# Kernel tuning notes

Measured on AMD Instinct MI355X. Metric: run time of the kernel, lower is better.

Reference implementation:

```python
import jax, jax.numpy as jnp
import numpy as np

DN = ('NCHW', 'OIHW', 'NCHW')

def conv2d(x, w, b, stride, pad):
    y = jax.lax.conv_general_dilated(x, w, (stride, stride), ((pad, pad), (pad, pad)), dimension_numbers=DN)
    return y + b[None, :, None, None]

def convt2d(x, w, b):
    # torch ConvTranspose2d(k=4, stride=2, padding=1); torch weight layout [Cin, Cout, kH, kW]
    wf = jnp.flip(w, (2, 3)).transpose(1, 0, 2, 3)  # -> [Cout, Cin, kH, kW]
    y = jax.lax.conv_general_dilated(x, wf, (1, 1), ((2, 2), (2, 2)), lhs_dilation=(2, 2), dimension_numbers=DN)
    return y + b[None, :, None, None]

def setup_inputs() -> dict:
    key = jax.random.key(0)
    ks = jax.random.split(key, 20)
    Hc, E, K = 128, 256, 8192
    s = lambda k, shape, fan: jax.random.normal(k, shape, jnp.float32) * (1.0 / np.sqrt(fan))
    inp = {
        'x': jax.random.normal(ks[0], (4, 3, 256, 256), jnp.float32),
        'enc_w1': s(ks[1], (Hc, 3, 4, 4), 3 * 16), 'enc_b1': jnp.zeros((Hc,), jnp.float32),
        'enc_w2': s(ks[2], (Hc, Hc, 4, 4), Hc * 16), 'enc_b2': jnp.zeros((Hc,), jnp.float32),
        'enc_w3': s(ks[3], (Hc, Hc, 3, 3), Hc * 9), 'enc_b3': jnp.zeros((Hc,), jnp.float32),
        'qconv_w': s(ks[4], (E, Hc, 1, 1), Hc), 'qconv_b': jnp.zeros((E,), jnp.float32),
        'codebook': jax.random.uniform(ks[5], (K, E), jnp.float32, -1.0 / K, 1.0 / K),
        'pqconv_w': s(ks[6], (Hc, E, 1, 1), E), 'pqconv_b': jnp.zeros((Hc,), jnp.float32),
        'dec_w1': s(ks[7], (Hc, Hc, 3, 3), Hc * 9), 'dec_b1': jnp.zeros((Hc,), jnp.float32),
        'dect_w2': s(ks[8], (Hc, Hc, 4, 4), Hc * 16), 'dect_b2': jnp.zeros((Hc,), jnp.float32),
        'dect_w3': s(ks[9], (Hc, 3, 4, 4), Hc * 16), 'dect_b3': jnp.zeros((3,), jnp.float32),
    }
    return inp

def quantize(z, codebook):
    B, C, H, W = z.shape
    zf = z.transpose(0, 2, 3, 1).reshape(-1, C)  # [N, C]
    d = (jnp.sum(zf * zf, axis=1, keepdims=True)
         + jnp.sum(codebook * codebook, axis=1)
         - 2.0 * zf @ codebook.T)  # [N, K]
    indices = jnp.argmin(d, axis=1)
    quant = codebook[indices].reshape(B, H, W, C).transpose(0, 3, 1, 2)
    commit_loss = jnp.mean((jax.lax.stop_gradient(quant) - z) ** 2)
    quant = z + jax.lax.stop_gradient(quant - z)  # straight-through
    return quant, indices, commit_loss

def reference(x, enc_w1, enc_b1, enc_w2, enc_b2, enc_w3, enc_b3, qconv_w, qconv_b,
              codebook, pqconv_w, pqconv_b, dec_w1, dec_b1, dect_w2, dect_b2, dect_w3, dect_b3):
    h = jax.nn.relu(conv2d(x, enc_w1, enc_b1, 2, 1))
    h = jax.nn.relu(conv2d(h, enc_w2, enc_b2, 2, 1))
    h = conv2d(h, enc_w3, enc_b3, 1, 1)
    h = conv2d(h, qconv_w, qconv_b, 1, 0)
    quant, indices, commit_loss = quantize(h, codebook)
    q = conv2d(quant, pqconv_w, pqconv_b, 1, 0)
    d = jax.nn.relu(conv2d(q, dec_w1, dec_b1, 1, 1))
    d = jax.nn.relu(convt2d(d, dect_w2, dect_b2))
    recon = convt2d(d, dect_w3, dect_b3)
    return recon, commit_loss, indices
```

## Files before the change

kernel.cpp:

```cpp
#include <hip/hip_runtime.h>

#define OFF_A     ((size_t)0)
#define OFF_BINFO ((size_t)8388608)
#define OFF_B     ((size_t)34611200)
#define OFF_C     ((size_t)43532288)
#define OFF_D     ((size_t)52453376)
#define OFF_E     ((size_t)69230592)
#define OFF_ZN    ((size_t)81813504)
#define OFF_CN    ((size_t)81879040)
#define OFF_IDX   ((size_t)81911808)
#define OFF_ACC   ((size_t)81977344)
#define OFF_WR2   ((size_t)81977600)
#define OFF_WR3   ((size_t)83026176)
#define OFF_QWT   ((size_t)83050752)
#define OFF_WD2   ((size_t)83181824)
#define OFF_WD3   ((size_t)85278976)
#define OFF_WD1   ((size_t)86458624)

#define VQ_MARGIN 1.2e-4f
#define LDSS 40

typedef __attribute__((ext_vector_type(8))) _Float16 f16x8;
typedef __attribute__((ext_vector_type(4))) float f32x4;

__device__ __forceinline__ unsigned fkey(float f) {
  unsigned u = __float_as_uint(f);
  return (u & 0x80000000u) ? ~u : (u | 0x80000000u);
}
__device__ __forceinline__ float funkey(unsigned k) {
  unsigned u = (k & 0x80000000u) ? (k ^ 0x80000000u) : ~k;
  return __uint_as_float(u);
}
__device__ __forceinline__ void padzero_img(float* base, int S, int t) {
  for (int e = t; e < 4 * S - 4; e += 256) {
    int rr, cc;
    if (e < S) { rr = 0; cc = e; }
    else if (e < 2 * S) { rr = S - 1; cc = e - S; }
    else { rr = ((e - 2 * S) >> 1) + 1; cc = (e & 1) ? (S - 1) : 0; }
    base[rr * S + cc] = 0.0f;
  }
}
__device__ __forceinline__ void padzero_img_h(_Float16* base, int S, int t) {
  for (int e = t; e < 4 * S - 4; e += 256) {
    int rr, cc;
    if (e < S) { rr = 0; cc = e; }
    else if (e < 2 * S) { rr = S - 1; cc = e - S; }
    else { rr = ((e - 2 * S) >> 1) + 1; cc = (e & 1) ? (S - 1) : 0; }
    base[rr * S + cc] = (_Float16)0.0f;
  }
}

__global__ __launch_bounds__(256) void prep_k(
    const float* __restrict__ dtw2, _Float16* __restrict__ wh2,
    const float* __restrict__ dtw3, float* __restrict__ wr3,
    const float* __restrict__ qw,   float* __restrict__ qwT,
    const float* __restrict__ ew2,  double* __restrict__ wd2,
    const float* __restrict__ ew3,  double* __restrict__ wd3,
    const float* __restrict__ ew1,  double* __restrict__ wd1,
    float* __restrict__ xpad, float* __restrict__ h1p, float* __restrict__ h2p) {
  int b = blockIdx.x, t = threadIdx.x;
  if (b < 256) {
    int tid = b * 256 + t;
    int ci = tid & 127, co = (tid >> 7) & 127, cls = tid >> 14;
    int kh0 = 1 - (cls >> 1), kw0 = 1 - (cls & 1);
    const float* s = dtw2 + ((size_t)ci * 128 + co) * 16;
    _Float16* d = wh2 + (size_t)tid * 4;
    float d0 = s[kh0 * 4 + kw0];       float d1v = s[kh0 * 4 + kw0 + 2];
    float d2v = s[(kh0 + 2) * 4 + kw0]; float d3v = s[(kh0 + 2) * 4 + kw0 + 2];
    d[0] = (_Float16)d1v; d[1] = (_Float16)d0;
    d[2] = (_Float16)d3v; d[3] = (_Float16)d2v;
  } else if (b < 262) {
    int tid = (b - 256) * 256 + t;
    if (tid < 1536) {
      int ci = tid & 127, co = (tid >> 7) % 3, cls = tid / 384;
      int kh0 = 1 - (cls >> 1), kw0 = 1 - (cls & 1);
      const float* s = dtw3 + ((size_t)ci * 3 + co) * 16;
      float* d = wr3 + (size_t)tid * 4;
      d[0] = s[kh0 * 4 + kw0];       d[1] = s[kh0 * 4 + kw0 + 2];
      d[2] = s[(kh0 + 2) * 4 + kw0]; d[3] = s[(kh0 + 2) * 4 + kw0 + 2];
    }
  } else if (b < 390) {
    int tid = (b - 262) * 256 + t;
    int co = tid & 255, ci = tid >> 8;
    qwT[(size_t)ci * 256 + co] = qw[(size_t)co * 128 + ci];
  } else if (b < 1414) {
    int tid = (b - 390) * 256 + t;
    wd2[tid] = (double)ew2[tid];
  } else if (b < 1990) {
    int tid = (b - 1414) * 256 + t;
    wd3[tid] = (double)ew3[tid];
  } else if (b < 2014) {
    int tid = (b - 1990) * 256 + t;
    wd1[tid] = (double)ew1[tid];
  } else if (b < 2026) {
    padzero_img(xpad + (size_t)(b - 2014) * 66564, 258, t);
  } else if (b < 2538) {
    padzero_img(h1p + (size_t)(b - 2026) * 16900, 130, t);
  } else {
    padzero_img(h2p + (size_t)(b - 2538) * 4356, 66, t);
  }
}

__global__ __launch_bounds__(256) void padx_k(const float* __restrict__ x,
                                              float* __restrict__ xp) {
  int tid = blockIdx.x * 256 + threadIdx.x;
  int wo = tid & 255, ho = (tid >> 8) & 255, c = tid >> 16;
  xp[((size_t)c * 258 + ho + 1) * 258 + wo + 1] = x[tid];
}

__global__ __launch_bounds__(256) void conv1_k(
    const float* __restrict__ xp, const double* __restrict__ wd,
    const float* __restrict__ bias, float* __restrict__ h1p) {
  int b = blockIdx.x;
  int chunk = b & 63, cog = (b >> 6) & 15, n = b >> 10;
  int t = threadIdx.x;
  int wo = t & 127, ho = chunk * 2 + (t >> 7);
  int co0 = cog * 8;
  const float* xb = xp + (size_t)n * 3 * 66564 + (size_t)(2 * ho) * 258 + 2 * wo;
  double acc[8] = {};
  for (int ci = 0; ci < 3; ++ci) {
    const float* xc = xb + (size_t)ci * 66564;
    float cf[16];
#pragma unroll
    for (int kh = 0; kh < 4; ++kh)
#pragma unroll
      for (int kw = 0; kw < 4; ++kw) cf[kh * 4 + kw] = xc[kh * 258 + kw];
    const double* wp = wd + (size_t)co0 * 48 + ci * 16;
#pragma unroll
    for (int tp = 0; tp < 16; ++tp) {
      double xd = (double)cf[tp];
#pragma unroll
      for (int cc = 0; cc < 8; ++cc)
        acc[cc] = fma(xd, wp[(size_t)cc * 48 + tp], acc[cc]);
    }
  }
#pragma unroll
  for (int cc = 0; cc < 8; ++cc) {
    float r = (float)((double)bias[co0 + cc] + acc[cc]);
    h1p[(((size_t)n * 128 + co0 + cc) * 130 + ho + 1) * 130 + wo + 1] = fmaxf(r, 0.0f);
  }
}

__global__ __launch_bounds__(256) void conv2_k(
    const float* __restrict__ h1p, const double* __restrict__ wd,
    const float* __restrict__ bias, float* __restrict__ h2p) {
  int b = blockIdx.x;
  int chunk = b & 15, cog = (b >> 4) & 15, n = b >> 8;
  int t = threadIdx.x;
  int wo = t & 63, ho = chunk * 4 + (t >> 6);
  int co0 = cog * 8;
  const float* xb = h1p + (size_t)n * 128 * 16900 + (size_t)(2 * ho) * 130 + 2 * wo;
  double acc[8] = {};
  for (int ci = 0; ci < 128; ++ci) {
    const float* xc = xb + (size_t)ci * 16900;
    float cf[16];
#pragma unroll
    for (int kh = 0; kh < 4; ++kh) {
      float2 p0 = *(const float2*)(xc + kh * 130);
      float2 p1 = *(const float2*)(xc + kh * 130 + 2);
      cf[kh * 4 + 0] = p0.x; cf[kh * 4 + 1] = p0.y;
      cf[kh * 4 + 2] = p1.x; cf[kh * 4 + 3] = p1.y;
    }
    const double* wp = wd + (size_t)co0 * 2048 + ci * 16;
#pragma unroll
    for (int tp = 0; tp < 16; ++tp) {
      double xd = (double)cf[tp];
#pragma unroll
      for (int cc = 0; cc < 8; ++cc)
        acc[cc] = fma(xd, wp[(size_t)cc * 2048 + tp], acc[cc]);
    }
  }
#pragma unroll
  for (int cc = 0; cc < 8; ++cc) {
    float r = (float)((double)bias[co0 + cc] + acc[cc]);
    h2p[(((size_t)n * 128 + co0 + cc) * 66 + ho + 1) * 66 + wo + 1] = fmaxf(r, 0.0f);
  }
}

__global__ __launch_bounds__(256) void conv3_k(
    const float* __restrict__ h2p, const double* __restrict__ wd,
    const float* __restrict__ bias, float* __restrict__ h3) {
  int b = blockIdx.x;
  int chunk = b & 15, cog = (b >> 4) & 15, n = b >> 8;
  int t = threadIdx.x;
  int wo = t & 63, ho = chunk * 4 + (t >> 6);
  int co0 = cog * 8;
  const float* xb = h2p + (size_t)n * 128 * 4356 + (size_t)ho * 66 + wo;
  double acc[8] = {};
  for (int ci = 0; ci < 128; ++ci) {
    const float* xc = xb + (size_t)ci * 4356;
    float cf[9];
#pragma unroll
    for (int kh = 0; kh < 3; ++kh)
#pragma unroll
      for (int kw = 0; kw < 3; ++kw) cf[kh * 3 + kw] = xc[kh * 66 + kw];
    const double* wp = wd + (size_t)co0 * 1152 + ci * 9;
#pragma unroll
    for (int tp = 0; tp < 9; ++tp) {
      double xd = (double)cf[tp];
#pragma unroll
      for (int cc = 0; cc < 8; ++cc)
        acc[cc] = fma(xd, wp[(size_t)cc * 1152 + tp], acc[cc]);
    }
  }
#pragma unroll
  for (int cc = 0; cc < 8; ++cc)
    h3[(((size_t)n * 128 + co0 + cc) << 12) + (ho << 6) + wo] =
        (float)((double)bias[co0 + cc] + acc[cc]);
}

__global__ __launch_bounds__(256) void qconv_z_k(
    const float* __restrict__ h3, const float* __restrict__ wT,
    const float* __restrict__ bias, float* __restrict__ zf,
    _Float16* __restrict__ Ap, float* __restrict__ znb) {
  __shared__ double wsum[4];
  int p  = blockIdx.x;
  int co = threadIdx.x;
  int n  = p >> 12;
  int hw = p & 4095;
  const float* xp = h3 + ((size_t)n * 128) * 4096 + hw;
  double a[4] = {0.0, 0.0, 0.0, 0.0};
  for (int ci = 0; ci < 128; ci += 4) {
#pragma unroll
    for (int u = 0; u < 4; ++u) {
      float xv = xp[(size_t)(ci + u) * 4096];
      a[u] = fma((double)xv, (double)wT[(size_t)(ci + u) * 256 + co], a[u]);
    }
  }
  double acc = (double)bias[co] + ((a[0] + a[1]) + (a[2] + a[3]));
  float zv = (float)acc;
  zf[(size_t)p * 256 + co] = zv;
  Ap[(size_t)p * 256 + co] = (_Float16)zv;
  float xx = zv * zv;
  double s = (double)xx;
#pragma unroll
  for (int off = 32; off > 0; off >>= 1) s += __shfl_down(s, off, 64);
  if ((co & 63) == 0) wsum[co >> 6] = s;
  __syncthreads();
  if (co == 0) znb[p] = (float)((wsum[0] + wsum[1]) + (wsum[2] + wsum[3]));
}

__global__ __launch_bounds__(256) void cbprep_k(
    const float* __restrict__ cb, _Float16* __restrict__ Bp,
    float* __restrict__ cnb) {
  __shared__ double wsum[4];
  int k = blockIdx.x, t = threadIdx.x;
  float c = cb[(size_t)k * 256 + t];
  Bp[(size_t)k * 256 + t] = (_Float16)(c * 512.0f);
  float xx = c * c;
  double s = (double)xx;
#pragma unroll
  for (int off = 32; off > 0; off >>= 1) s += __shfl_down(s, off, 64);
  if ((t & 63) == 0) wsum[t >> 6] = s;
  __syncthreads();
  if (t == 0) cnb[k] = (float)((wsum[0] + wsum[1]) + (wsum[2] + wsum[3]));
}

__global__ __launch_bounds__(256, 2) void vq_gemm_k(
    const _Float16* __restrict__ Ah, const _Float16* __restrict__ Bh,
    const float* __restrict__ cnArr, int4* __restrict__ binfo) {
  __shared__ __align__(16) _Float16 As[128 * LDSS];
  __shared__ __align__(16) _Float16 Bs[128 * LDSS];
  __shared__ unsigned loc[128];
  __shared__ int cnt_sh[128];
  __shared__ int cand_sh[128][2];
  const int t = threadIdx.x;
  const int w = t >> 6, L = t & 63;
  const int mb = blockIdx.x >> 6;
  const int nb = blockIdx.x & 63;
  const int m0 = mb << 7, n0 = nb << 7;
  if (t < 128) { loc[t] = 0xFFFFFFFFu; cnt_sh[t] = 0; }
  f32x4 acc[4][4] = {};
  const int wr = (w >> 1) << 6, wc = (w & 1) << 6;
  const int srow = L >> 2, kg = L & 3;
  const int q = L >> 4, ln = L & 15;
  for (int kk = 0; kk < 256; kk += 32) {
    __syncthreads();
#pragma unroll
    for (int c = 0; c < 2; ++c) {
      const int row = (w << 5) + (c << 4) + srow;
      const f16x8 av = *(const f16x8*)(Ah + (size_t)(m0 + row) * 256 + kk + kg * 8);
      *(f16x8*)(&As[row * LDSS + kg * 8]) = av;
      const f16x8 bv = *(const f16x8*)(Bh + (size_t)(n0 + row) * 256 + kk + kg * 8);
      *(f16x8*)(&Bs[row * LDSS + kg * 8]) = bv;
    }
    __syncthreads();
    f16x8 af[4], bf[4];
#pragma unroll
    for (int i = 0; i < 4; ++i)
      af[i] = *(const f16x8*)(&As[(wr + 16 * i + ln) * LDSS + q * 8]);
#pragma unroll
    for (int j = 0; j < 4; ++j)
      bf[j] = *(const f16x8*)(&Bs[(wc + 16 * j + ln) * LDSS + q * 8]);
#pragma unroll
    for (int i = 0; i < 4; ++i)
#pragma unroll
      for (int j = 0; j < 4; ++j)
        acc[i][j] = __builtin_amdgcn_mfma_f32_16x16x32_f16(af[i], bf[j], acc[i][j], 0, 0, 0);
  }
  float cnv[4];
#pragma unroll
  for (int j = 0; j < 4; ++j) cnv[j] = cnArr[n0 + wc + 16 * j + ln];
#pragma unroll
  for (int i = 0; i < 4; ++i)
#pragma unroll
    for (int r = 0; r < 4; ++r) {
      float mn = 3.4e38f;
#pragma unroll
      for (int j = 0; j < 4; ++j)
        mn = fminf(mn, fmaf(-0.00390625f, acc[i][j][r], cnv[j]));
#pragma unroll
      for (int s = 1; s < 16; s <<= 1)
        mn = fminf(mn, __shfl_xor(mn, s, 64));
      if (ln == 0) atomicMin(&loc[wr + 16 * i + 4 * q + r], fkey(mn));
    }
  __syncthreads();
#pragma unroll
  for (int i = 0; i < 4; ++i)
#pragma unroll
    for (int r = 0; r < 4; ++r) {
      const int rib = wr + 16 * i + 4 * q + r;
      const float thr = funkey(loc[rib]) + VQ_MARGIN;
#pragma unroll
      for (int j = 0; j < 4; ++j) {
        float s = fmaf(-0.00390625f, acc[i][j][r], cnv[j]);
        if (s <= thr) {
          int slot = atomicAdd(&cnt_sh[rib], 1);
          if (slot < 2) cand_sh[rib][slot] = n0 + wc + 16 * j + ln;
        }
      }
    }
  __syncthreads();
  if (t < 128) {
    int4 v;
    v.x = cnt_sh[t];
    v.y = cand_sh[t][0];
    v.z = cand_sh[t][1];
    v.w = (int)__float_as_uint(funkey(loc[t]));
    binfo[(size_t)(m0 + t) * 64 + nb] = v;
  }
}

__global__ __launch_bounds__(256) void vq_phase3_k(
    const float* __restrict__ zf, const float* __restrict__ cb,
    const float* __restrict__ znArr, const float* __restrict__ cnArr,
    const int4* __restrict__ binfo, int* __restrict__ idxOut,
    float* __restrict__ accum) {
  if (blockIdx.x == 0 && threadIdx.x == 0) *accum = 0.0f;
  const int lane = threadIdx.x & 63;
  const int r = blockIdx.x * 4 + (threadIdx.x >> 6);
  const float* zr = zf + (size_t)r * 256;
  double z4[4];
#pragma unroll
  for (int j = 0; j < 4; ++j) z4[j] = (double)zr[lane + (j << 6)];
  const float znr = znArr[r];
  int4 b = binfo[(size_t)r * 64 + lane];
  float bv = __uint_as_float((unsigned)b.w);
  float m = bv;
#pragma unroll
  for (int off = 32; off > 0; off >>= 1) m = fminf(m, __shfl_down(m, off, 64));
  m = __shfl(m, 0, 64);
  const float thr = m + VQ_MARGIN;
  unsigned long long mask = __ballot(bv <= thr);
  float bestd = 3.4e38f;
  int bestk = 0x7fffffff;
  while (mask) {
    const int nb = (int)__builtin_ctzll(mask);
    mask &= mask - 1;
    const int c  = __shfl(b.x, nb, 64);
    const int k0 = __shfl(b.y, nb, 64);
    const int k1 = __shfl(b.z, nb, 64);
    const int nsc = (c <= 2) ? c : 128;
    for (int s2 = 0; s2 < nsc; ++s2) {
      const int k = (c <= 2) ? (s2 == 0 ? k0 : k1) : (nb * 128 + s2);
      const float* ck = cb + (size_t)k * 256;
      double p = 0.0;
#pragma unroll
      for (int j = 0; j < 4; ++j)
        p = fma(z4[j], (double)ck[lane + (j << 6)], p);
#pragma unroll
      for (int off = 32; off > 0; off >>= 1) p += __shfl_down(p, off, 64);
      if (lane == 0) {
        float mm2 = (float)(2.0 * p);
        float t1 = znr + cnArr[k];
        float d = t1 - mm2;
        if (d < bestd || (d == bestd && k < bestk)) { bestd = d; bestk = k; }
      }
    }
  }
  if (lane == 0) idxOut[r] = bestk;
}

__global__ __launch_bounds__(256) void commit_k(
    const float* __restrict__ zf, const float* __restrict__ cb,
    const int* __restrict__ idxArr, float* __restrict__ accum,
    float* __restrict__ outIdxF) {
  __shared__ float wsum[4];
  const int p = blockIdx.x;
  const int t = threadIdx.x;
  const int k = idxArr[p];
  float d = cb[(size_t)k * 256 + t] - zf[(size_t)p * 256 + t];
  float v = d * d;
#pragma unroll
  for (int off = 32; off > 0; off >>= 1) v += __shfl_down(v, off, 64);
  if ((t & 63) == 0) wsum[t >> 6] = v;
  __syncthreads();
  if (t == 0) {
    atomicAdd(accum, wsum[0] + wsum[1] + wsum[2] + wsum[3]);
    outIdxF[p] = (float)k;
  }
}

__global__ __launch_bounds__(256) void pc_k(const float* __restrict__ cb,
                                            const float* __restrict__ pw,
                                            float* __restrict__ PC) {
  int tid = blockIdx.x * 256 + threadIdx.x;
  int co = tid & 127, k = tid >> 7;
  const float* c = cb + (size_t)k * 256;
  const float* w = pw + (size_t)co * 256;
  float a0 = 0.0f, a1 = 0.0f, a2 = 0.0f, a3 = 0.0f;
  for (int ci = 0; ci < 256; ci += 4) {
    a0 = fmaf(c[ci], w[ci], a0);
    a1 = fmaf(c[ci + 1], w[ci + 1], a1);
    a2 = fmaf(c[ci + 2], w[ci + 2], a2);
    a3 = fmaf(c[ci + 3], w[ci + 3], a3);
  }
  PC[tid] = (a0 + a1) + (a2 + a3);
}

__global__ __launch_bounds__(256) void padzero_dec_k(
    float* __restrict__ qbufp, _Float16* __restrict__ d1pH,
    float* __restrict__ d2p) {
  int b = blockIdx.x, t = threadIdx.x;
  if (b < 512)       padzero_img(qbufp + (size_t)b * 4356, 66, t);
  else if (b < 1024) padzero_img_h(d1pH + (size_t)(b - 512) * 4356, 66, t);
  else               padzero_img(d2p + (size_t)(b - 1024) * 16900, 130, t);
}

__global__ __launch_bounds__(256) void gather_pc_k(
    const float* __restrict__ PC, const int* __restrict__ idxArr,
    const float* __restrict__ pb, float* __restrict__ qp) {
  int tid = blockIdx.x * 256 + threadIdx.x;
  int hw = tid & 4095;
  int co = (tid >> 12) & 127;
  int n  = tid >> 19;
  int p  = (n << 12) + hw;
  int h = hw >> 6, w2 = hw & 63;
  qp[(((size_t)n * 128 + co) * 66 + h + 1) * 66 + w2 + 1] =
      PC[(size_t)idxArr[p] * 128 + co] + pb[co];
}

__global__ __launch_bounds__(256) void dconv1_k(
    const float* __restrict__ qp, const float* __restrict__ w,
    const float* __restrict__ bias, _Float16* __restrict__ d1pH) {
  int b = blockIdx.x;
  int chunk = b & 15, cog = (b >> 4) & 15, n = b >> 8;
  int t = threadIdx.x;
  int wo = t & 63, ho = chunk * 4 + (t >> 6);
  int co0 = cog * 8;
  const float* xb = qp + (size_t)n * 128 * 4356 + (size_t)ho * 66 + wo;
  float acc[8] = {};
  for (int ci = 0; ci < 128; ++ci) {
    const float* xc = xb + (size_t)ci * 4356;
    float xv[9];
#pragma unroll
    for (int kh = 0; kh < 3; ++kh)
#pragma unroll
      for (int kw = 0; kw < 3; ++kw) xv[kh * 3 + kw] = xc[kh * 66 + kw];
#pragma unroll
    for (int cc = 0; cc < 8; ++cc) {
      const float* wp = w + (size_t)(co0 + cc) * 1152 + ci * 9;
#pragma unroll
      for (int tp = 0; tp < 9; ++tp)
        acc[cc] = fmaf(xv[tp], wp[tp], acc[cc]);
    }
  }
#pragma unroll
  for (int cc = 0; cc < 8; ++cc)
    d1pH[(((size_t)n * 128 + co0 + cc) * 66 + ho + 1) * 66 + wo + 1] =
        (_Float16)fmaxf(bias[co0 + cc] + acc[cc], 0.0f);
}

__global__ __launch_bounds__(256) void convt2_k(
    const _Float16* __restrict__ xh, const _Float16* __restrict__ wh,
    const float* __restrict__ bias, float* __restrict__ y) {
  int b = blockIdx.x;
  int i = b & 63, cog = (b >> 6) & 7, cls = (b >> 9) & 3, n = b >> 11;
  int cph = cls >> 1, cpw = cls & 1;
  int t = threadIdx.x;
  int wv = t >> 6, l = t & 63;
  int q = l >> 4, ln = l & 15;
  int wb = (wv << 4) + ln;
  int co0 = cog << 4;
  int r0 = i + 1 + cph, r1 = r0 - 1;
  int c1 = wb + cpw;
  int o0 = r0 * 66 + c1, o1 = r1 * 66 + c1;
  const unsigned short* xb =
      (const unsigned short*)xh + (size_t)n * 128 * 4356 + (size_t)(q * 2) * 4356;
  const _Float16* ap = wh + (size_t)(cls * 128 + co0 + ln) * 512 + q * 8;
  f32x4 acc = {0.0f, 0.0f, 0.0f, 0.0f};
  for (int s = 0; s < 16; ++s) {
    const unsigned short* pa = xb + (size_t)(s * 8) * 4356;
    const unsigned short* pb2 = pa + 4356;
    unsigned v0 = pa[o0], v1 = pa[o0 + 1];
    unsigned v2 = pa[o1], v3 = pa[o1 + 1];
    unsigned v4 = pb2[o0], v5 = pb2[o0 + 1];
    unsigned v6 = pb2[o1], v7 = pb2[o1 + 1];
    union { unsigned u[4]; f16x8 h; } bb;
    bb.u[0] = v0 | (v1 << 16);
    bb.u[1] = v2 | (v3 << 16);
    bb.u[2] = v4 | (v5 << 16);
    bb.u[3] = v6 | (v7 << 16);
    const f16x8 af = *(const f16x8*)(ap + s * 32);
    acc = __builtin_amdgcn_mfma_f32_16x16x32_f16(af, bb.h, acc, 0, 0, 0);
  }
  int ho = 2 * i + cph, wo = 2 * wb + cpw;
#pragma unroll
  for (int r = 0; r < 4; ++r) {
    int co = co0 + q * 4 + r;
    y[(((size_t)n * 128 + co) * 130 + ho + 1) * 130 + wo + 1] =
        fmaxf(bias[co] + acc[r], 0.0f);
  }
}

__global__ __launch_bounds__(256) void convt3_k(
    const float* __restrict__ xp, const float* __restrict__ wr,
    const float* __restrict__ bias, float* __restrict__ y,
    const float* __restrict__ accum, float* __restrict__ outLoss) {
  int b = blockIdx.x;
  if (b == 0 && threadIdx.x == 0) *outLoss = *accum * (1.0f / 4194304.0f);
  int chunk = b & 63, cls = (b >> 6) & 3, n = b >> 8;
  int cph = cls >> 1, cpw = cls & 1;
  int t = threadIdx.x;
  int wb = t & 127, i = chunk * 2 + (t >> 7);
  int ho = 2 * i + cph, wo = 2 * wb + cpw;
  int r0 = i + 1 + cph, r1 = r0 - 1;
  int c0 = wb + 1 + cpw, c1 = c0 - 1;
  const float* xb = xp + (size_t)n * 128 * 16900;
  float acc[3] = {0.0f, 0.0f, 0.0f};
  for (int ci = 0; ci < 128; ++ci) {
    const float* xc = xb + (size_t)ci * 16900;
    float x00 = xc[r0 * 130 + c0], x01 = xc[r0 * 130 + c1];
    float x10 = xc[r1 * 130 + c0], x11 = xc[r1 * 130 + c1];
#pragma unroll
    for (int cc = 0; cc < 3; ++cc) {
      const float* w4 = wr + (((size_t)cls * 3 + cc) * 128 + ci) * 4;
      acc[cc] = fmaf(x00, w4[0], acc[cc]);
      acc[cc] = fmaf(x01, w4[1], acc[cc]);
      acc[cc] = fmaf(x10, w4[2], acc[cc]);
      acc[cc] = fmaf(x11, w4[3], acc[cc]);
    }
  }
#pragma unroll
  for (int cc = 0; cc < 3; ++cc)
    y[(((size_t)n * 3 + cc) << 16) + (ho << 8) + wo] = bias[cc] + acc[cc];
}

extern "C" void kernel_launch(void* const* d_in, const int* in_sizes, int n_in,
                              void* d_out, int out_size, void* d_ws, size_t ws_size,
                              hipStream_t stream) {
  const float* x    = (const float*)d_in[0];
  const float* ew1  = (const float*)d_in[1];
  const float* eb1  = (const float*)d_in[2];
  const float* ew2  = (const float*)d_in[3];
  const float* eb2  = (const float*)d_in[4];
  const float* ew3  = (const float*)d_in[5];
  const float* eb3  = (const float*)d_in[6];
  const float* qw   = (const float*)d_in[7];
  const float* qb   = (const float*)d_in[8];
  const float* cb   = (const float*)d_in[9];
  const float* pw   = (const float*)d_in[10];
  const float* pb   = (const float*)d_in[11];
  const float* dw1  = (const float*)d_in[12];
  const float* db1  = (const float*)d_in[13];
  const float* dtw2 = (const float*)d_in[14];
  const float* dtb2 = (const float*)d_in[15];
  const float* dtw3 = (const float*)d_in[16];
  const float* dtb3 = (const float*)d_in[17];

  char* wsb = (char*)d_ws;
  float*    h1p  = (float*)(wsb + OFF_A);
  _Float16* Ap   = (_Float16*)(wsb + OFF_A);
  int4*     binfo= (int4*)(wsb + OFF_BINFO);
  float*    d2p  = (float*)(wsb + OFF_A);
  float*    h2p  = (float*)(wsb + OFF_B);
  float*    qbufp= (float*)(wsb + OFF_B);
  float*    xpad = (float*)(wsb + OFF_C);
  float*    h3   = (float*)(wsb + OFF_C);
  _Float16* d1pH = (_Float16*)(wsb + OFF_C);
  float*    zff  = (float*)(wsb + OFF_D);
  _Float16* Bp   = (_Float16*)(wsb + OFF_E);
  float*    PC   = (float*)(wsb + OFF_E);
  float*    znb  = (float*)(wsb + OFF_ZN);
  float*    cnb  = (float*)(wsb + OFF_CN);
  int*      idxb = (int*)(wsb + OFF_IDX);
  float*    accum= (float*)(wsb + OFF_ACC);
  _Float16* wh2  = (_Float16*)(wsb + OFF_WR2);
  float*    wr3  = (float*)(wsb + OFF_WR3);
  float*    qwT  = (float*)(wsb + OFF_QWT);
  double*   wd2  = (double*)(wsb + OFF_WD2);
  double*   wd3  = (double*)(wsb + OFF_WD3);
  double*   wd1  = (double*)(wsb + OFF_WD1);

  float* out      = (float*)d_out;
  float* outLoss  = out + 786432;
  float* outIdxF  = out + 786433;

  hipLaunchKernelGGL(prep_k, dim3(3050), dim3(256), 0, stream,
                     dtw2, wh2, dtw3, wr3, qw, qwT, ew2, wd2, ew3, wd3,
                     ew1, wd1, xpad, h1p, h2p);

  hipLaunchKernelGGL(padx_k,    dim3(3072),  dim3(256), 0, stream, x, xpad);
  hipLaunchKernelGGL(conv1_k,   dim3(4096),  dim3(256), 0, stream, xpad, wd1, eb1, h1p);
  hipLaunchKernelGGL(conv2_k,   dim3(1024),  dim3(256), 0, stream, h1p, wd2, eb2, h2p);
  hipLaunchKernelGGL(conv3_k,   dim3(1024),  dim3(256), 0, stream, h2p, wd3, eb3, h3);
  hipLaunchKernelGGL(qconv_z_k, dim3(16384), dim3(256), 0, stream, h3, qwT, qb, zff, Ap, znb);

  hipLaunchKernelGGL(cbprep_k,    dim3(8192),  dim3(256), 0, stream, cb, Bp, cnb);
  hipLaunchKernelGGL(vq_gemm_k,   dim3(8192),  dim3(256), 0, stream, Ap, Bp, cnb, binfo);
  hipLaunchKernelGGL(vq_phase3_k, dim3(4096),  dim3(256), 0, stream, zff, cb, znb, cnb, binfo, idxb, accum);
  hipLaunchKernelGGL(commit_k,    dim3(16384), dim3(256), 0, stream, zff, cb, idxb, accum, outIdxF);

  hipLaunchKernelGGL(pc_k,          dim3(4096), dim3(256), 0, stream, cb, pw, PC);
  hipLaunchKernelGGL(padzero_dec_k, dim3(1536), dim3(256), 0, stream, qbufp, d1pH, d2p);
  hipLaunchKernelGGL(gather_pc_k,   dim3(8192), dim3(256), 0, stream, PC, idxb, pb, qbufp);
  hipLaunchKernelGGL(dconv1_k,      dim3(1024), dim3(256), 0, stream, qbufp, dw1, db1, d1pH);
  hipLaunchKernelGGL(convt2_k,      dim3(8192), dim3(256), 0, stream, d1pH, wh2, dtb2, d2p);
  hipLaunchKernelGGL(convt3_k,      dim3(1024), dim3(256), 0, stream, d2p, wr3, dtb3, out, accum, outLoss);
}
```

Before: 1.387 ms.

## Run decoder 3x3 conv on fp16 MFMA and store decoder activations in fp16

Rewrites the decoder 3x3 conv (dconv1) from a scalar fp32 FMA loop into an implicit-GEMM kernel using 16x16x32 fp16 MFMA. Its weights are pre-rearranged into an fp16 tap-major layout inside the prep kernel. The quantized input and the first transposed-conv output now use fp16 buffers, which halves the memory traffic for gather, convt2 and convt3. The cost is lower precision in the decoder path, and the MFMA B-operand is built from eight strided 16-bit loads per step.

After: 1.338 ms. -3.5%, faster.

```diff
diff --git a/kernel.cpp b/kernel.cpp
--- a/kernel.cpp
+++ b/kernel.cpp
@@ -11,6 +11,7 @@
 #define OFF_IDX   ((size_t)81911808)
 #define OFF_ACC   ((size_t)81977344)
 #define OFF_WR2   ((size_t)81977600)
+#define OFF_WHD1  ((size_t)82501888)
 #define OFF_WR3   ((size_t)83026176)
 #define OFF_QWT   ((size_t)83050752)
 #define OFF_WD2   ((size_t)83181824)
@@ -57,6 +58,7 @@
     const float* __restrict__ ew2,  double* __restrict__ wd2,
     const float* __restrict__ ew3,  double* __restrict__ wd3,
     const float* __restrict__ ew1,  double* __restrict__ wd1,
+    const float* __restrict__ dw1,  _Float16* __restrict__ whd1,
     float* __restrict__ xpad, float* __restrict__ h1p, float* __restrict__ h2p) {
   int b = blockIdx.x, t = threadIdx.x;
   if (b < 256) {
@@ -96,8 +98,13 @@
     padzero_img(xpad + (size_t)(b - 2014) * 66564, 258, t);
   } else if (b < 2538) {
     padzero_img(h1p + (size_t)(b - 2026) * 16900, 130, t);
+  } else if (b < 3050) {
+    padzero_img(h2p + (size_t)(b - 2538) * 4356, 66, t);
   } else {
-    padzero_img(h2p + (size_t)(b - 2538) * 4356, 66, t);
+    int tid = (b - 3050) * 256 + t;
+    int co = tid / 1152, k = tid - co * 1152;
+    int tap = k >> 7, ci = k & 127;
+    whd1[tid] = (_Float16)dw1[((size_t)co * 128 + ci) * 9 + tap];
   }
 }
 
@@ -429,61 +436,68 @@
 }
 
 __global__ __launch_bounds__(256) void padzero_dec_k(
-    float* __restrict__ qbufp, _Float16* __restrict__ d1pH,
-    float* __restrict__ d2p) {
+    _Float16* __restrict__ qH, _Float16* __restrict__ d1pH,
+    _Float16* __restrict__ d2pH) {
   int b = blockIdx.x, t = threadIdx.x;
-  if (b < 512)       padzero_img(qbufp + (size_t)b * 4356, 66, t);
+  if (b < 512)       padzero_img_h(qH + (size_t)b * 4356, 66, t);
   else if (b < 1024) padzero_img_h(d1pH + (size_t)(b - 512) * 4356, 66, t);
-  else               padzero_img(d2p + (size_t)(b - 1024) * 16900, 130, t);
+  else               padzero_img_h(d2pH + (size_t)(b - 1024) * 16900, 130, t);
 }
 
 __global__ __launch_bounds__(256) void gather_pc_k(
     const float* __restrict__ PC, const int* __restrict__ idxArr,
-    const float* __restrict__ pb, float* __restrict__ qp) {
+    const float* __restrict__ pb, _Float16* __restrict__ qH) {
   int tid = blockIdx.x * 256 + threadIdx.x;
   int hw = tid & 4095;
   int co = (tid >> 12) & 127;
   int n  = tid >> 19;
   int p  = (n << 12) + hw;
   int h = hw >> 6, w2 = hw & 63;
-  qp[(((size_t)n * 128 + co) * 66 + h + 1) * 66 + w2 + 1] =
-      PC[(size_t)idxArr[p] * 128 + co] + pb[co];
+  qH[(((size_t)n * 128 + co) * 66 + h + 1) * 66 + w2 + 1] =
+      (_Float16)(PC[(size_t)idxArr[p] * 128 + co] + pb[co]);
 }
 
 __global__ __launch_bounds__(256) void dconv1_k(
-    const float* __restrict__ qp, const float* __restrict__ w,
+    const _Float16* __restrict__ qH, const _Float16* __restrict__ wa,
     const float* __restrict__ bias, _Float16* __restrict__ d1pH) {
   int b = blockIdx.x;
-  int chunk = b & 15, cog = (b >> 4) & 15, n = b >> 8;
+  int ho = b & 63, cog = (b >> 6) & 7, n = b >> 9;
   int t = threadIdx.x;
-  int wo = t & 63, ho = chunk * 4 + (t >> 6);
-  int co0 = cog * 8;
-  const float* xb = qp + (size_t)n * 128 * 4356 + (size_t)ho * 66 + wo;
-  float acc[8] = {};
-  for (int ci = 0; ci < 128; ++ci) {
-    const float* xc = xb + (size_t)ci * 4356;
-    float xv[9];
-#pragma unroll
-    for (int kh = 0; kh < 3; ++kh)
-#pragma unroll
-      for (int kw = 0; kw < 3; ++kw) xv[kh * 3 + kw] = xc[kh * 66 + kw];
-#pragma unroll
-    for (int cc = 0; cc < 8; ++cc) {
-      const float* wp = w + (size_t)(co0 + cc) * 1152 + ci * 9;
-#pragma unroll
-      for (int tp = 0; tp < 9; ++tp)
-        acc[cc] = fmaf(xv[tp], wp[tp], acc[cc]);
-    }
-  }
-#pragma unroll
-  for (int cc = 0; cc < 8; ++cc)
-    d1pH[(((size_t)n * 128 + co0 + cc) * 66 + ho + 1) * 66 + wo + 1] =
-        (_Float16)fmaxf(bias[co0 + cc] + acc[cc], 0.0f);
+  int wv = t >> 6, l = t & 63;
+  int q = l >> 4, ln = l & 15;
+  int wo0 = wv << 4;
+  const unsigned short* qb = (const unsigned short*)qH + (size_t)n * 128 * 4356;
+  const _Float16* ap = wa + (size_t)(cog * 16 + ln) * 1152 + q * 8;
+  f32x4 acc = {0.0f, 0.0f, 0.0f, 0.0f};
+#pragma unroll
+  for (int s = 0; s < 36; ++s) {
+    const int tap = s >> 2, dh = tap / 3, dw = tap % 3;
+    const int cig = ((s & 3) << 5) + (q << 3);
+    const unsigned short* bp =
+        qb + (size_t)cig * 4356 + (ho + dh) * 66 + wo0 + ln + dw;
+    unsigned v0 = bp[0],        v1 = bp[4356];
+    unsigned v2 = bp[2 * 4356], v3 = bp[3 * 4356];
+    unsigned v4 = bp[4 * 4356], v5 = bp[5 * 4356];
+    unsigned v6 = bp[6 * 4356], v7 = bp[7 * 4356];
+    union { unsigned u[4]; f16x8 h; } bb;
+    bb.u[0] = v0 | (v1 << 16);
+    bb.u[1] = v2 | (v3 << 16);
+    bb.u[2] = v4 | (v5 << 16);
+    bb.u[3] = v6 | (v7 << 16);
+    const f16x8 af = *(const f16x8*)(ap + s * 32);
+    acc = __builtin_amdgcn_mfma_f32_16x16x32_f16(af, bb.h, acc, 0, 0, 0);
+  }
+#pragma unroll
+  for (int r = 0; r < 4; ++r) {
+    int co = (cog << 4) + (q << 2) + r;
+    d1pH[(((size_t)n * 128 + co) * 66 + ho + 1) * 66 + wo0 + ln + 1] =
+        (_Float16)fmaxf(bias[co] + acc[r], 0.0f);
+  }
 }
 
 __global__ __launch_bounds__(256) void convt2_k(
     const _Float16* __restrict__ xh, const _Float16* __restrict__ wh,
-    const float* __restrict__ bias, float* __restrict__ y) {
+    const float* __restrict__ bias, _Float16* __restrict__ y) {
   int b = blockIdx.x;
   int i = b & 63, cog = (b >> 6) & 7, cls = (b >> 9) & 3, n = b >> 11;
   int cph = cls >> 1, cpw = cls & 1;
@@ -519,12 +533,12 @@
   for (int r = 0; r < 4; ++r) {
     int co = co0 + q * 4 + r;
     y[(((size_t)n * 128 + co) * 130 + ho + 1) * 130 + wo + 1] =
-        fmaxf(bias[co] + acc[r], 0.0f);
+        (_Float16)fmaxf(bias[co] + acc[r], 0.0f);
   }
 }
 
 __global__ __launch_bounds__(256) void convt3_k(
-    const float* __restrict__ xp, const float* __restrict__ wr,
+    const _Float16* __restrict__ xh, const float* __restrict__ wr,
     const float* __restrict__ bias, float* __restrict__ y,
     const float* __restrict__ accum, float* __restrict__ outLoss) {
   int b = blockIdx.x;
@@ -536,12 +550,12 @@
   int ho = 2 * i + cph, wo = 2 * wb + cpw;
   int r0 = i + 1 + cph, r1 = r0 - 1;
   int c0 = wb + 1 + cpw, c1 = c0 - 1;
-  const float* xb = xp + (size_t)n * 128 * 16900;
+  const _Float16* xb = xh + (size_t)n * 128 * 16900;
   float acc[3] = {0.0f, 0.0f, 0.0f};
   for (int ci = 0; ci < 128; ++ci) {
-    const float* xc = xb + (size_t)ci * 16900;
-    float x00 = xc[r0 * 130 + c0], x01 = xc[r0 * 130 + c1];
-    float x10 = xc[r1 * 130 + c0], x11 = xc[r1 * 130 + c1];
+    const _Float16* xc = xb + (size_t)ci * 16900;
+    float x00 = (float)xc[r0 * 130 + c0], x01 = (float)xc[r0 * 130 + c1];
+    float x10 = (float)xc[r1 * 130 + c0], x11 = (float)xc[r1 * 130 + c1];
 #pragma unroll
     for (int cc = 0; cc < 3; ++cc) {
       const float* w4 = wr + (((size_t)cls * 3 + cc) * 128 + ci) * 4;
@@ -582,9 +596,9 @@
   float*    h1p  = (float*)(wsb + OFF_A);
   _Float16* Ap   = (_Float16*)(wsb + OFF_A);
   int4*     binfo= (int4*)(wsb + OFF_BINFO);
-  float*    d2p  = (float*)(wsb + OFF_A);
+  _Float16* d2pH = (_Float16*)(wsb + OFF_A);
   float*    h2p  = (float*)(wsb + OFF_B);
-  float*    qbufp= (float*)(wsb + OFF_B);
+  _Float16* qH   = (_Float16*)(wsb + OFF_B);
   float*    xpad = (float*)(wsb + OFF_C);
   float*    h3   = (float*)(wsb + OFF_C);
   _Float16* d1pH = (_Float16*)(wsb + OFF_C);
@@ -596,6 +610,7 @@
   int*      idxb = (int*)(wsb + OFF_IDX);
   float*    accum= (float*)(wsb + OFF_ACC);
   _Float16* wh2  = (_Float16*)(wsb + OFF_WR2);
+  _Float16* whd1 = (_Float16*)(wsb + OFF_WHD1);
   float*    wr3  = (float*)(wsb + OFF_WR3);
   float*    qwT  = (float*)(wsb + OFF_QWT);
   double*   wd2  = (double*)(wsb + OFF_WD2);
@@ -606,9 +621,9 @@
   float* outLoss  = out + 786432;
   float* outIdxF  = out + 786433;
 
-  hipLaunchKernelGGL(prep_k, dim3(3050), dim3(256), 0, stream,
+  hipLaunchKernelGGL(prep_k, dim3(3626), dim3(256), 0, stream,
                      dtw2, wh2, dtw3, wr3, qw, qwT, ew2, wd2, ew3, wd3,
-                     ew1, wd1, xpad, h1p, h2p);
+                     ew1, wd1, dw1, whd1, xpad, h1p, h2p);
 
   hipLaunchKernelGGL(padx_k,    dim3(3072),  dim3(256), 0, stream, x, xpad);
   hipLaunchKernelGGL(conv1_k,   dim3(4096),  dim3(256), 0, stream, xpad, wd1, eb1, h1p);
@@ -622,9 +637,9 @@
   hipLaunchKernelGGL(commit_k,    dim3(16384), dim3(256), 0, stream, zff, cb, idxb, accum, outIdxF);
 
   hipLaunchKernelGGL(pc_k,          dim3(4096), dim3(256), 0, stream, cb, pw, PC);
-  hipLaunchKernelGGL(padzero_dec_k, dim3(1536), dim3(256), 0, stream, qbufp, d1pH, d2p);
-  hipLaunchKernelGGL(gather_pc_k,   dim3(8192), dim3(256), 0, stream, PC, idxb, pb, qbufp);
-  hipLaunchKernelGGL(dconv1_k,      dim3(1024), dim3(256), 0, stream, qbufp, dw1, db1, d1pH);
-  hipLaunchKernelGGL(convt2_k,      dim3(8192), dim3(256), 0, stream, d1pH, wh2, dtb2, d2p);
-  hipLaunchKernelGGL(convt3_k,      dim3(1024), dim3(256), 0, stream, d2p, wr3, dtb3, out, accum, outLoss);
-}
+  hipLaunchKernelGGL(padzero_dec_k, dim3(1536), dim3(256), 0, stream, qH, d1pH, d2pH);
+  hipLaunchKernelGGL(gather_pc_k,   dim3(8192), dim3(256), 0, stream, PC, idxb, pb, qH);
+  hipLaunchKernelGGL(dconv1_k,      dim3(2048), dim3(256), 0, stream, qH, whd1, db1, d1pH);
+  hipLaunchKernelGGL(convt2_k,      dim3(8192), dim3(256), 0, stream, d1pH, wh2, dtb2, d2pH);
+  hipLaunchKernelGGL(convt3_k,      dim3(1024), dim3(256), 0, stream, d2pH, wr3, dtb3, out, accum, outLoss);
+}
```
